# Optimization experiments

Hardware: AMD Instinct MI355X
Metric: run time of the kernel (lower is better)

Reference implementation:

```python
import math
import jax, jax.numpy as jnp
import numpy as np

D = 512
H = 8
HD = D // H
FF = 2048
EPS = 1e-5


def _layernorm(x, gamma, beta):
    mean = jnp.mean(x, axis=-1, keepdims=True)
    var = jnp.mean((x - mean) ** 2, axis=-1, keepdims=True)
    return gamma * (x - mean) / jnp.sqrt(var + EPS) + beta


def _attention(q, k, v, mask):
    # q,k,v: [B,H,Sq/Sk,hd]; mask: [B,Sq,Sk] additive, broadcast over heads
    scale = 1.0 / math.sqrt(q.shape[-1])
    scores = jnp.einsum('bhqd,bhkd->bhqk', q, k) * scale
    scores = scores + mask[:, None, :, :]
    probs = jax.nn.softmax(scores, axis=-1)
    return jnp.einsum('bhqk,bhkd->bhqd', probs, v)


def setup_inputs() -> dict:
    key = jax.random.key(0)
    ks = jax.random.split(key, 20)
    B, S_ENC, S_DEC = 256, 512, 64
    s = 0.02
    inp = {
        'x': jax.random.normal(ks[0], (B, S_ENC, D), jnp.float32),
        'y': jax.random.normal(ks[1], (B, S_DEC, D), jnp.float32),
        'mask': jnp.zeros((B, S_DEC, S_DEC), jnp.float32),
        'mask2': jnp.zeros((B, S_DEC, S_ENC), jnp.float32),
        # self-attention params
        'qkv_w': jax.random.normal(ks[2], (D, 3 * D), jnp.float32) * s,
        'qkv_b': jnp.zeros((3 * D,), jnp.float32),
        'sa_out_w': jax.random.normal(ks[3], (D, D), jnp.float32) * s,
        'sa_out_b': jnp.zeros((D,), jnp.float32),
        # cross-attention params
        'q_w': jax.random.normal(ks[4], (D, D), jnp.float32) * s,
        'q_b': jnp.zeros((D,), jnp.float32),
        'kv_w': jax.random.normal(ks[5], (D, 2 * D), jnp.float32) * s,
        'kv_b': jnp.zeros((2 * D,), jnp.float32),
        'ca_out_w': jax.random.normal(ks[6], (D, D), jnp.float32) * s,
        'ca_out_b': jnp.zeros((D,), jnp.float32),
        # ffn params
        'l1_w': jax.random.normal(ks[7], (D, FF), jnp.float32) * s,
        'l1_b': jnp.zeros((FF,), jnp.float32),
        'l2_w': jax.random.normal(ks[8], (FF, D), jnp.float32) * s,
        'l2_b': jnp.zeros((D,), jnp.float32),
        # layernorm params
        'g1': jnp.ones((D,), jnp.float32), 'b1': jnp.zeros((D,), jnp.float32),
        'g2': jnp.ones((D,), jnp.float32), 'b2': jnp.zeros((D,), jnp.float32),
        'g3': jnp.ones((D,), jnp.float32), 'b3': jnp.zeros((D,), jnp.float32),
    }
    return inp


def reference(x, y, mask, mask2, qkv_w, qkv_b, sa_out_w, sa_out_b,
              q_w, q_b, kv_w, kv_b, ca_out_w, ca_out_b,
              l1_w, l1_b, l2_w, l2_b, g1, b1, g2, b2, g3, b3):
    B, Sd, _ = y.shape
    Se = x.shape[1]

    # --- self attention (post-norm, dropout is identity at eval) ---
    resid = y
    qkv = y @ qkv_w + qkv_b                     # [B,Sd,3D]
    qkv = qkv.reshape(B, Sd, H, 3 * HD).transpose(0, 2, 1, 3)
    q, k, v = jnp.split(qkv, 3, axis=-1)        # each [B,H,Sd,hd]
    vals = _attention(q, k, v, mask)
    vals = vals.transpose(0, 2, 1, 3).reshape(B, Sd, D)
    y = vals @ sa_out_w + sa_out_b
    y = _layernorm(y + resid, g1, b1)

    # --- cross attention: kv from encoder x, q from decoder y ---
    resid = y
    kv = x @ kv_w + kv_b                        # [B,Se,2D]
    kv = kv.reshape(B, Se, H, 2 * HD).transpose(0, 2, 1, 3)
    k, v = jnp.split(kv, 2, axis=-1)            # each [B,H,Se,hd]
    q = (y @ q_w + q_b).reshape(B, Sd, H, HD).transpose(0, 2, 1, 3)
    vals = _attention(q, k, v, mask2)
    vals = vals.transpose(0, 2, 1, 3).reshape(B, Sd, D)
    y = vals @ ca_out_w + ca_out_b
    y = _layernorm(y + resid, g2, b2)

    # --- feed forward ---
    resid = y
    h = jax.nn.relu(y @ l1_w + l1_b)
    y = h @ l2_w + l2_b
    y = _layernorm(y + resid, g3, b3)
    return y
```

## Files before the change

### kernel.cpp

```cpp
#include <hip/hip_runtime.h>
#include <hip/hip_bf16.h>
#include <stdint.h>


#define SDEC 64
#define SENC 512
#define DMODEL 512
#define FFDIM 2048

typedef __bf16 bf16x8 __attribute__((ext_vector_type(8)));
typedef float  f32x4  __attribute__((ext_vector_type(4)));

static __device__ __forceinline__ float bf2f(unsigned short u) {
  union { unsigned int i; float f; } w; w.i = ((unsigned int)u) << 16; return w.f;
}
static __device__ __forceinline__ unsigned short f2bf(float f) {
  union { float f; unsigned int i; } w; w.f = f;
  unsigned int u = w.i;
  return (unsigned short)((u + 0x7fffu + ((u >> 16) & 1u)) >> 16);
}

static __device__ __forceinline__ void gl_lds16(const unsigned short* g, unsigned short* l) {
  __builtin_amdgcn_global_load_lds(
      (const __attribute__((address_space(1))) unsigned int*)g,
      (__attribute__((address_space(3))) unsigned int*)l,
      16, 0, 0);
}

__global__ __launch_bounds__(256)
void cvt_f32_bf16(const float* __restrict__ in, unsigned short* __restrict__ out, size_t n8)
{
  size_t i = (size_t)blockIdx.x * blockDim.x + threadIdx.x;
  const size_t stride = (size_t)gridDim.x * blockDim.x;
  for (; i < n8; i += stride) {
    const float* p = in + i * 8;
    float4 a = *(const float4*)p, b = *(const float4*)(p + 4);
    union { unsigned short s[8]; uint4 v; } u;
    u.s[0] = f2bf(a.x); u.s[1] = f2bf(a.y); u.s[2] = f2bf(a.z); u.s[3] = f2bf(a.w);
    u.s[4] = f2bf(b.x); u.s[5] = f2bf(b.y); u.s[6] = f2bf(b.z); u.s[7] = f2bf(b.w);
    *(uint4*)(out + i * 8) = u.v;
  }
}

template<int A_F32, int RELU, int OUT_F32>
__global__ __launch_bounds__(256, 2)
void gemm_kernel(const void* __restrict__ Aptr, const unsigned short* __restrict__ Bt,
                 const float* __restrict__ bias, void* __restrict__ Cptr,
                 int M, int N, int K)
{
  __shared__ unsigned short As[128 * 32];
  __shared__ unsigned short Bs[128 * 32];
  const int tid  = threadIdx.x;
  const int row0 = blockIdx.y * 128;
  const int col0 = blockIdx.x * 128;
  const int w    = tid >> 6, lane = tid & 63;
  const int wm   = w >> 1, wn = w & 1;
  const int gr   = lane >> 2;
  const int gc   = (lane & 3) * 8;
  const int srow = tid >> 2;
  const int scol = (tid & 3) * 8;

  f32x4 acc[4][4];
  #pragma unroll
  for (int i = 0; i < 4; ++i)
    #pragma unroll
    for (int j = 0; j < 4; ++j)
      acc[i][j] = (f32x4){0.f, 0.f, 0.f, 0.f};

  for (int k0 = 0; k0 < K; k0 += 32) {
    __syncthreads();
    if (A_F32) {
      const float* A = (const float*)Aptr;
      #pragma unroll
      for (int c = 0; c < 2; ++c) {
        const int r = srow + c * 64;
        const float* src = A + (size_t)(row0 + r) * K + (k0 + scol);
        float4 f0 = *(const float4*)src;
        float4 f1 = *(const float4*)(src + 4);
        union { unsigned short s[8]; uint4 v; } p;
        p.s[0] = f2bf(f0.x); p.s[1] = f2bf(f0.y); p.s[2] = f2bf(f0.z); p.s[3] = f2bf(f0.w);
        p.s[4] = f2bf(f1.x); p.s[5] = f2bf(f1.y); p.s[6] = f2bf(f1.z); p.s[7] = f2bf(f1.w);
        *(uint4*)&As[r * 32 + scol] = p.v;
      }
    } else {
      const unsigned short* A = (const unsigned short*)Aptr;
      #pragma unroll
      for (int i = 0; i < 2; ++i) {
        const int rbase = w * 32 + i * 16;
        gl_lds16(A + (size_t)(row0 + rbase + gr) * K + (k0 + gc), &As[rbase * 32]);
      }
    }
    #pragma unroll
    for (int i = 0; i < 2; ++i) {
      const int rbase = w * 32 + i * 16;
      gl_lds16(Bt + (size_t)(col0 + rbase + gr) * K + (k0 + gc), &Bs[rbase * 32]);
    }
    __syncthreads();

    const int fr = lane & 15, fk = (lane >> 4) * 8;
    bf16x8 af[4], bfr[4];
    #pragma unroll
    for (int mi = 0; mi < 4; ++mi)
      af[mi] = *(const bf16x8*)&As[(wm * 64 + mi * 16 + fr) * 32 + fk];
    #pragma unroll
    for (int ni = 0; ni < 4; ++ni)
      bfr[ni] = *(const bf16x8*)&Bs[(wn * 64 + ni * 16 + fr) * 32 + fk];
    #pragma unroll
    for (int mi = 0; mi < 4; ++mi)
      #pragma unroll
      for (int ni = 0; ni < 4; ++ni)
        acc[mi][ni] = __builtin_amdgcn_mfma_f32_16x16x32_bf16(af[mi], bfr[ni], acc[mi][ni], 0, 0, 0);
  }

  const int fr = lane & 15, fq = lane >> 4;
  #pragma unroll
  for (int ni = 0; ni < 4; ++ni) {
    const int c = col0 + wn * 64 + ni * 16 + fr;
    const float bv = bias ? bias[c] : 0.f;
    #pragma unroll
    for (int mi = 0; mi < 4; ++mi) {
      #pragma unroll
      for (int t = 0; t < 4; ++t) {
        const int r = row0 + wm * 64 + mi * 16 + fq * 4 + t;
        float v = acc[mi][ni][t] + bv;
        if (RELU) v = fmaxf(v, 0.f);
        if (OUT_F32) ((float*)Cptr)[(size_t)r * N + c] = v;
        else ((unsigned short*)Cptr)[(size_t)r * N + c] = f2bf(v);
      }
    }
  }
}

__global__ __launch_bounds__(256, 2)
void attn_mfma(const unsigned short* __restrict__ qbuf, int qstride, int qmul,
               const unsigned short* __restrict__ kvbuf, int kvstride, int kmul, int kadd,
               int tokmul, int Skv, const float* __restrict__ mask,
               unsigned short* __restrict__ vals, float scale)
{
  __shared__ unsigned short Qs[64 * 72];
  __shared__ unsigned short Ks[64 * 72];
  __shared__ unsigned short Vt[64 * 72];
  __shared__ unsigned short Ps[64 * 72];

  const int h = blockIdx.x, b = blockIdx.y;
  const int tid = threadIdx.x;
  const int w = tid >> 6, lane = tid & 63;
  const int srow = tid >> 2;
  const int sc0 = (tid & 3) * 16;

  {
    const unsigned short* qg = qbuf + (size_t)(b * 64 + srow) * qstride + h * qmul + sc0;
    *(uint4*)&Qs[srow * 72 + sc0]     = *(const uint4*)qg;
    *(uint4*)&Qs[srow * 72 + sc0 + 8] = *(const uint4*)(qg + 8);
  }

  const int fr = lane & 15;
  const int fg = lane >> 4;
  const int orow = fg * 4;

  float mstate[4], lstate[4];
  f32x4 oacc[4];
  #pragma unroll
  for (int t = 0; t < 4; ++t) { mstate[t] = -1e30f; lstate[t] = 0.f; }
  #pragma unroll
  for (int ni = 0; ni < 4; ++ni) oacc[ni] = (f32x4){0.f, 0.f, 0.f, 0.f};

  for (int j0 = 0; j0 < Skv; j0 += 64) {
    __syncthreads();
    {
      const unsigned short* kg = kvbuf + (size_t)(b * tokmul + j0 + srow) * kvstride
                                 + h * kmul + kadd + sc0;
      *(uint4*)&Ks[srow * 72 + sc0]     = *(const uint4*)kg;
      *(uint4*)&Ks[srow * 72 + sc0 + 8] = *(const uint4*)(kg + 8);
      const unsigned short* vg = kg + 64;
      uint4 v0 = *(const uint4*)vg;
      uint4 v1 = *(const uint4*)(vg + 8);
      const unsigned short* vsp = (const unsigned short*)&v0;
      #pragma unroll
      for (int jj = 0; jj < 8; ++jj) Vt[(sc0 + jj) * 72 + srow] = vsp[jj];
      vsp = (const unsigned short*)&v1;
      #pragma unroll
      for (int jj = 0; jj < 8; ++jj) Vt[(sc0 + 8 + jj) * 72 + srow] = vsp[jj];
    }
    __syncthreads();

    f32x4 s[4];
    #pragma unroll
    for (int ni = 0; ni < 4; ++ni) s[ni] = (f32x4){0.f, 0.f, 0.f, 0.f};
    #pragma unroll
    for (int ks = 0; ks < 2; ++ks) {
      bf16x8 aq = *(const bf16x8*)&Qs[(w * 16 + fr) * 72 + ks * 32 + fg * 8];
      #pragma unroll
      for (int ni = 0; ni < 4; ++ni) {
        bf16x8 bk = *(const bf16x8*)&Ks[(ni * 16 + fr) * 72 + ks * 32 + fg * 8];
        s[ni] = __builtin_amdgcn_mfma_f32_16x16x32_bf16(aq, bk, s[ni], 0, 0, 0);
      }
    }

    #pragma unroll
    for (int t = 0; t < 4; ++t) {
      const int grow = w * 16 + orow + t;
      const float* mrow = mask + ((size_t)b * 64 + grow) * Skv + j0;
      float sv[4];
      float tmax = -1e30f;
      #pragma unroll
      for (int ni = 0; ni < 4; ++ni) {
        sv[ni] = s[ni][t] * scale + mrow[ni * 16 + fr];
        tmax = fmaxf(tmax, sv[ni]);
      }
      #pragma unroll
      for (int off = 1; off < 16; off <<= 1) tmax = fmaxf(tmax, __shfl_xor(tmax, off));
      const float mn = fmaxf(mstate[t], tmax);
      const float fscl = __expf(mstate[t] - mn);
      mstate[t] = mn;
      float psum = 0.f;
      #pragma unroll
      for (int ni = 0; ni < 4; ++ni) {
        float p = __expf(sv[ni] - mn);
        psum += p;
        Ps[grow * 72 + ni * 16 + fr] = f2bf(p);
      }
      #pragma unroll
      for (int off = 1; off < 16; off <<= 1) psum += __shfl_xor(psum, off);
      lstate[t] = lstate[t] * fscl + psum;
      #pragma unroll
      for (int ni = 0; ni < 4; ++ni) oacc[ni][t] *= fscl;
    }
    __syncthreads();

    #pragma unroll
    for (int ks = 0; ks < 2; ++ks) {
      bf16x8 pa = *(const bf16x8*)&Ps[(w * 16 + fr) * 72 + ks * 32 + fg * 8];
      #pragma unroll
      for (int ni = 0; ni < 4; ++ni) {
        bf16x8 vb = *(const bf16x8*)&Vt[(ni * 16 + fr) * 72 + ks * 32 + fg * 8];
        oacc[ni] = __builtin_amdgcn_mfma_f32_16x16x32_bf16(pa, vb, oacc[ni], 0, 0, 0);
      }
    }
  }

  #pragma unroll
  for (int t = 0; t < 4; ++t) {
    const int grow = w * 16 + orow + t;
    const float inv = 1.f / lstate[t];
    unsigned short* og = vals + (size_t)(b * 64 + grow) * DMODEL + h * 64;
    #pragma unroll
    for (int ni = 0; ni < 4; ++ni)
      og[ni * 16 + fr] = f2bf(oacc[ni][t] * inv);
  }
}

__global__ __launch_bounds__(256)
void ln_kernel(const float* __restrict__ proj, const float* __restrict__ resid32,
               const unsigned short* __restrict__ resid16,
               const float* __restrict__ gamma, const float* __restrict__ beta,
               unsigned short* __restrict__ out16, float* __restrict__ out32)
{
  const int w = threadIdx.x >> 6, lane = threadIdx.x & 63;
  const size_t r = (size_t)blockIdx.x * 4 + w;
  const int d0 = lane * 8;

  float x[8];
  {
    const float* p = proj + r * DMODEL + d0;
    float4 a = *(const float4*)p, b = *(const float4*)(p + 4);
    x[0] = a.x; x[1] = a.y; x[2] = a.z; x[3] = a.w;
    x[4] = b.x; x[5] = b.y; x[6] = b.z; x[7] = b.w;
  }
  if (resid32) {
    const float* p = resid32 + r * DMODEL + d0;
    float4 a = *(const float4*)p, b = *(const float4*)(p + 4);
    x[0] += a.x; x[1] += a.y; x[2] += a.z; x[3] += a.w;
    x[4] += b.x; x[5] += b.y; x[6] += b.z; x[7] += b.w;
  } else {
    uint4 u = *(const uint4*)(resid16 + r * DMODEL + d0);
    const unsigned short* s = (const unsigned short*)&u;
    #pragma unroll
    for (int j = 0; j < 8; ++j) x[j] += bf2f(s[j]);
  }

  float sum = 0.f;
  #pragma unroll
  for (int j = 0; j < 8; ++j) sum += x[j];
  #pragma unroll
  for (int off = 32; off > 0; off >>= 1) sum += __shfl_xor(sum, off);
  const float mean = sum * (1.f / DMODEL);

  float vs = 0.f;
  #pragma unroll
  for (int j = 0; j < 8; ++j) { float t = x[j] - mean; vs += t * t; }
  #pragma unroll
  for (int off = 32; off > 0; off >>= 1) vs += __shfl_xor(vs, off);
  const float rstd = rsqrtf(vs * (1.f / DMODEL) + 1e-5f);

  float4 g0 = *(const float4*)(gamma + d0), g1 = *(const float4*)(gamma + d0 + 4);
  float4 b0 = *(const float4*)(beta + d0),  b1 = *(const float4*)(beta + d0 + 4);
  const float g[8]  = {g0.x, g0.y, g0.z, g0.w, g1.x, g1.y, g1.z, g1.w};
  const float bb[8] = {b0.x, b0.y, b0.z, b0.w, b1.x, b1.y, b1.z, b1.w};
  float y[8];
  #pragma unroll
  for (int j = 0; j < 8; ++j) y[j] = g[j] * (x[j] - mean) * rstd + bb[j];

  if (out16) {
    union { unsigned short s[8]; uint4 v; } p;
    #pragma unroll
    for (int j = 0; j < 8; ++j) p.s[j] = f2bf(y[j]);
    *(uint4*)(out16 + r * DMODEL + d0) = p.v;
  }
  if (out32) {
    float* o = out32 + r * DMODEL + d0;
    *(float4*)o       = (float4){y[0], y[1], y[2], y[3]};
    *(float4*)(o + 4) = (float4){y[4], y[5], y[6], y[7]};
  }
}

__global__ __launch_bounds__(256)
void transpose_cvt(const float* __restrict__ W, unsigned short* __restrict__ Wt,
                   int K, int N)
{
  __shared__ float tile[32][33];
  const int tx = threadIdx.x, ty = threadIdx.y;
  const int n = blockIdx.x * 32 + tx;
  #pragma unroll
  for (int rr = 0; rr < 4; ++rr) {
    const int k = blockIdx.y * 32 + ty + rr * 8;
    tile[ty + rr * 8][tx] = W[(size_t)k * N + n];
  }
  __syncthreads();
  const int k2 = blockIdx.y * 32 + tx;
  #pragma unroll
  for (int rr = 0; rr < 4; ++rr) {
    const int n2 = blockIdx.x * 32 + ty + rr * 8;
    Wt[(size_t)n2 * K + k2] = f2bf(tile[tx][ty + rr * 8]);
  }
}

extern "C" void kernel_launch(void* const* d_in, const int* in_sizes, int n_in,
                              void* d_out, int out_size, void* d_ws, size_t ws_size,
                              hipStream_t stream)
{
  const float* x        = (const float*)d_in[0];
  const float* y        = (const float*)d_in[1];
  const float* mask     = (const float*)d_in[2];
  const float* mask2    = (const float*)d_in[3];
  const float* qkv_w    = (const float*)d_in[4];
  const float* qkv_b    = (const float*)d_in[5];
  const float* sa_out_w = (const float*)d_in[6];
  const float* sa_out_b = (const float*)d_in[7];
  const float* q_w      = (const float*)d_in[8];
  const float* q_b      = (const float*)d_in[9];
  const float* kv_w     = (const float*)d_in[10];
  const float* kv_b     = (const float*)d_in[11];
  const float* ca_out_w = (const float*)d_in[12];
  const float* ca_out_b = (const float*)d_in[13];
  const float* l1_w     = (const float*)d_in[14];
  const float* l1_b     = (const float*)d_in[15];
  const float* l2_w     = (const float*)d_in[16];
  const float* l2_b     = (const float*)d_in[17];
  const float* g1 = (const float*)d_in[18];
  const float* b1 = (const float*)d_in[19];
  const float* g2 = (const float*)d_in[20];
  const float* b2 = (const float*)d_in[21];
  const float* g3 = (const float*)d_in[22];
  const float* b3 = (const float*)d_in[23];

  const int B  = in_sizes[1] / (SDEC * DMODEL);
  const int M  = B * SDEC;
  const int ME = B * SENC;

  char* ws = (char*)d_ws;
  size_t off = 0;
  auto alloc = [&](size_t bytes) -> char* {
    char* p = ws + off;
    off += (bytes + 255) & ~(size_t)255;
    return p;
  };
  unsigned short* qkv_wt = (unsigned short*)alloc((size_t)1536 * 512 * 2);
  unsigned short* sa_wt  = (unsigned short*)alloc((size_t)512 * 512 * 2);
  unsigned short* q_wt   = (unsigned short*)alloc((size_t)512 * 512 * 2);
  unsigned short* kv_wt  = (unsigned short*)alloc((size_t)1024 * 512 * 2);
  unsigned short* ca_wt  = (unsigned short*)alloc((size_t)512 * 512 * 2);
  unsigned short* l1_wt  = (unsigned short*)alloc((size_t)2048 * 512 * 2);
  unsigned short* l2_wt  = (unsigned short*)alloc((size_t)512 * 2048 * 2);
  unsigned short* kvb    = (unsigned short*)alloc((size_t)ME * 1024 * 2);
  char*           xreg   = alloc((size_t)ME * 512 * 2);
  unsigned short* xb     = (unsigned short*)xreg;
  unsigned short* qkvb   = (unsigned short*)xreg;
  unsigned short* qb     = (unsigned short*)xreg;
  unsigned short* y2b    = (unsigned short*)(xreg + (size_t)16777216);
  unsigned short* valsb  = (unsigned short*)(xreg + (size_t)50331648);
  float*          proj   = (float*)(xreg + (size_t)67108864);
  unsigned short* y1b    = (unsigned short*)(xreg + (size_t)100663296);
  unsigned short* hb     = kvb;
  (void)ws_size; (void)n_in; (void)out_size;

  dim3 tb(32, 8);
  transpose_cvt<<<dim3(1536 / 32, 512 / 32), tb, 0, stream>>>(qkv_w, qkv_wt, 512, 1536);
  transpose_cvt<<<dim3(512 / 32, 512 / 32), tb, 0, stream>>>(sa_out_w, sa_wt, 512, 512);
  transpose_cvt<<<dim3(512 / 32, 512 / 32), tb, 0, stream>>>(q_w, q_wt, 512, 512);
  transpose_cvt<<<dim3(1024 / 32, 512 / 32), tb, 0, stream>>>(kv_w, kv_wt, 512, 1024);
  transpose_cvt<<<dim3(512 / 32, 512 / 32), tb, 0, stream>>>(ca_out_w, ca_wt, 512, 512);
  transpose_cvt<<<dim3(2048 / 32, 512 / 32), tb, 0, stream>>>(l1_w, l1_wt, 512, 2048);
  transpose_cvt<<<dim3(512 / 32, 2048 / 32), tb, 0, stream>>>(l2_w, l2_wt, 2048, 512);

  const float scale = 0.125f;

  cvt_f32_bf16<<<4096, 256, 0, stream>>>(x, xb, (size_t)ME * 512 / 8);
  gemm_kernel<0, 0, 0><<<dim3(1024 / 128, ME / 128), 256, 0, stream>>>(xb, kv_wt, kv_b, kvb, ME, 1024, 512);

  gemm_kernel<1, 0, 0><<<dim3(1536 / 128, M / 128), 256, 0, stream>>>(y, qkv_wt, qkv_b, qkvb, M, 1536, 512);
  attn_mfma<<<dim3(8, B), 256, 0, stream>>>(qkvb, 1536, 192, qkvb, 1536, 192, 64, SDEC, SDEC, mask, valsb, scale);
  gemm_kernel<0, 0, 1><<<dim3(512 / 128, M / 128), 256, 0, stream>>>(valsb, sa_wt, sa_out_b, proj, M, 512, 512);
  ln_kernel<<<M / 4, 256, 0, stream>>>(proj, y, nullptr, g1, b1, y1b, nullptr);

  gemm_kernel<0, 0, 0><<<dim3(512 / 128, M / 128), 256, 0, stream>>>(y1b, q_wt, q_b, qb, M, 512, 512);
  attn_mfma<<<dim3(8, B), 256, 0, stream>>>(qb, 512, 64, kvb, 1024, 128, 0, SENC, SENC, mask2, valsb, scale);
  gemm_kernel<0, 0, 1><<<dim3(512 / 128, M / 128), 256, 0, stream>>>(valsb, ca_wt, ca_out_b, proj, M, 512, 512);
  ln_kernel<<<M / 4, 256, 0, stream>>>(proj, nullptr, y1b, g2, b2, y2b, nullptr);

  gemm_kernel<0, 1, 0><<<dim3(2048 / 128, M / 128), 256, 0, stream>>>(y2b, l1_wt, l1_b, hb, M, 2048, 512);
  gemm_kernel<0, 0, 1><<<dim3(512 / 128, M / 128), 256, 0, stream>>>(hb, l2_wt, l2_b, proj, M, 512, 2048);
  ln_kernel<<<M / 4, 256, 0, stream>>>(proj, nullptr, y2b, g3, b3, nullptr, (float*)d_out);
}
```

Measured before the change: 730.5 us.

## Double-buffer GEMM loads, swizzle workgroups, stage bf16 epilogue via LDS

The GEMM now double-buffers its LDS tiles, issuing the next K-slice's global-to-LDS loads before computing on the current one. Workgroups are remapped (XCD-style swizzle) in both the GEMM and attention kernels. The GEMM epilogue writes through LDS so global stores are coalesced 16-byte vectors. Projection outputs become bf16 instead of fp32, which halves traffic into the layernorm kernels but costs precision before the residual add and layernorm. The fp32-A path is dropped; y is converted to bf16 by a separate kernel.

```diff
diff --git a/kernel.cpp b/kernel.cpp
--- a/kernel.cpp
+++ b/kernel.cpp
@@ -42,23 +42,39 @@
   }
 }
 
-template<int A_F32, int RELU, int OUT_F32>
+template<int RELU>
 __global__ __launch_bounds__(256, 2)
-void gemm_kernel(const void* __restrict__ Aptr, const unsigned short* __restrict__ Bt,
-                 const float* __restrict__ bias, void* __restrict__ Cptr,
+void gemm_kernel(const unsigned short* __restrict__ A, const unsigned short* __restrict__ Bt,
+                 const float* __restrict__ bias, unsigned short* __restrict__ C,
                  int M, int N, int K)
 {
-  __shared__ unsigned short As[128 * 32];
-  __shared__ unsigned short Bs[128 * 32];
-  const int tid  = threadIdx.x;
-  const int row0 = blockIdx.y * 128;
-  const int col0 = blockIdx.x * 128;
-  const int w    = tid >> 6, lane = tid & 63;
-  const int wm   = w >> 1, wn = w & 1;
-  const int gr   = lane >> 2;
-  const int gc   = (lane & 3) * 8;
-  const int srow = tid >> 2;
-  const int scol = (tid & 3) * 8;
+  __shared__ unsigned short sh[4 * 128 * 32];
+  const int tid = threadIdx.x;
+
+  const int gx   = gridDim.x;
+  const int nwg  = gx * gridDim.y;
+  const int orig = blockIdx.y * gx + blockIdx.x;
+  const int wg   = (orig & 7) * (nwg >> 3) + (orig >> 3);
+  const int row0 = (wg / gx) * 128;
+  const int col0 = (wg % gx) * 128;
+
+  const int w = tid >> 6, lane = tid & 63;
+  const int wm = w >> 1, wn = w & 1;
+  const int gr = lane >> 2, gc = (lane & 3) * 8;
+
+  unsigned short* As0 = sh;
+  unsigned short* Bs0 = sh + 8192;
+
+  auto STAGE = [&](int k0, int buf) {
+    unsigned short* as = As0 + buf * 4096;
+    unsigned short* bs = Bs0 + buf * 4096;
+    #pragma unroll
+    for (int i = 0; i < 2; ++i) {
+      const int rbase = w * 32 + i * 16;
+      gl_lds16(A  + (size_t)(row0 + rbase + gr) * K + (k0 + gc), as + rbase * 32);
+      gl_lds16(Bt + (size_t)(col0 + rbase + gr) * K + (k0 + gc), bs + rbase * 32);
+    }
+  };
 
   f32x4 acc[4][4];
   #pragma unroll
@@ -67,66 +83,81 @@
     for (int j = 0; j < 4; ++j)
       acc[i][j] = (f32x4){0.f, 0.f, 0.f, 0.f};
 
-  for (int k0 = 0; k0 < K; k0 += 32) {
-    __syncthreads();
-    if (A_F32) {
-      const float* A = (const float*)Aptr;
-      #pragma unroll
-      for (int c = 0; c < 2; ++c) {
-        const int r = srow + c * 64;
-        const float* src = A + (size_t)(row0 + r) * K + (k0 + scol);
-        float4 f0 = *(const float4*)src;
-        float4 f1 = *(const float4*)(src + 4);
-        union { unsigned short s[8]; uint4 v; } p;
-        p.s[0] = f2bf(f0.x); p.s[1] = f2bf(f0.y); p.s[2] = f2bf(f0.z); p.s[3] = f2bf(f0.w);
-        p.s[4] = f2bf(f1.x); p.s[5] = f2bf(f1.y); p.s[6] = f2bf(f1.z); p.s[7] = f2bf(f1.w);
-        *(uint4*)&As[r * 32 + scol] = p.v;
-      }
-    } else {
-      const unsigned short* A = (const unsigned short*)Aptr;
-      #pragma unroll
-      for (int i = 0; i < 2; ++i) {
-        const int rbase = w * 32 + i * 16;
-        gl_lds16(A + (size_t)(row0 + rbase + gr) * K + (k0 + gc), &As[rbase * 32]);
-      }
-    }
-    #pragma unroll
-    for (int i = 0; i < 2; ++i) {
-      const int rbase = w * 32 + i * 16;
-      gl_lds16(Bt + (size_t)(col0 + rbase + gr) * K + (k0 + gc), &Bs[rbase * 32]);
-    }
-    __syncthreads();
-
-    const int fr = lane & 15, fk = (lane >> 4) * 8;
+  const int fr = lane & 15, fk = (lane >> 4) * 8;
+
+  STAGE(0, 0);
+  int cur = 0;
+  for (int k0 = 0; k0 + 32 < K; k0 += 32) {
+    STAGE(k0 + 32, cur ^ 1);
+    asm volatile("s_waitcnt vmcnt(4)" ::: "memory");
+    __builtin_amdgcn_s_barrier();
+    asm volatile("" ::: "memory");
+    {
+      const unsigned short* as = As0 + cur * 4096;
+      const unsigned short* bs = Bs0 + cur * 4096;
+      bf16x8 af[4], bfr[4];
+      #pragma unroll
+      for (int mi = 0; mi < 4; ++mi)
+        af[mi] = *(const bf16x8*)&as[(wm * 64 + mi * 16 + fr) * 32 + fk];
+      #pragma unroll
+      for (int ni = 0; ni < 4; ++ni)
+        bfr[ni] = *(const bf16x8*)&bs[(wn * 64 + ni * 16 + fr) * 32 + fk];
+      #pragma unroll
+      for (int mi = 0; mi < 4; ++mi)
+        #pragma unroll
+        for (int ni = 0; ni < 4; ++ni)
+          acc[mi][ni] = __builtin_amdgcn_mfma_f32_16x16x32_bf16(af[mi], bfr[ni], acc[mi][ni], 0, 0, 0);
+    }
+    asm volatile("" ::: "memory");
+    __builtin_amdgcn_s_barrier();
+    cur ^= 1;
+  }
+  asm volatile("s_waitcnt vmcnt(0)" ::: "memory");
+  __builtin_amdgcn_s_barrier();
+  asm volatile("" ::: "memory");
+  {
+    const unsigned short* as = As0 + cur * 4096;
+    const unsigned short* bs = Bs0 + cur * 4096;
     bf16x8 af[4], bfr[4];
     #pragma unroll
     for (int mi = 0; mi < 4; ++mi)
-      af[mi] = *(const bf16x8*)&As[(wm * 64 + mi * 16 + fr) * 32 + fk];
+      af[mi] = *(const bf16x8*)&as[(wm * 64 + mi * 16 + fr) * 32 + fk];
     #pragma unroll
     for (int ni = 0; ni < 4; ++ni)
-      bfr[ni] = *(const bf16x8*)&Bs[(wn * 64 + ni * 16 + fr) * 32 + fk];
+      bfr[ni] = *(const bf16x8*)&bs[(wn * 64 + ni * 16 + fr) * 32 + fk];
     #pragma unroll
     for (int mi = 0; mi < 4; ++mi)
       #pragma unroll
       for (int ni = 0; ni < 4; ++ni)
         acc[mi][ni] = __builtin_amdgcn_mfma_f32_16x16x32_bf16(af[mi], bfr[ni], acc[mi][ni], 0, 0, 0);
   }
-
-  const int fr = lane & 15, fq = lane >> 4;
-  #pragma unroll
-  for (int ni = 0; ni < 4; ++ni) {
-    const int c = col0 + wn * 64 + ni * 16 + fr;
-    const float bv = bias ? bias[c] : 0.f;
-    #pragma unroll
-    for (int mi = 0; mi < 4; ++mi) {
-      #pragma unroll
-      for (int t = 0; t < 4; ++t) {
-        const int r = row0 + wm * 64 + mi * 16 + fq * 4 + t;
-        float v = acc[mi][ni][t] + bv;
-        if (RELU) v = fmaxf(v, 0.f);
-        if (OUT_F32) ((float*)Cptr)[(size_t)r * N + c] = v;
-        else ((unsigned short*)Cptr)[(size_t)r * N + c] = f2bf(v);
+  asm volatile("" ::: "memory");
+  __builtin_amdgcn_s_barrier();
+
+  {
+    const int fq = lane >> 4;
+    #pragma unroll
+    for (int ni = 0; ni < 4; ++ni) {
+      const int c = wn * 64 + ni * 16 + fr;
+      const float bv = bias ? bias[col0 + c] : 0.f;
+      #pragma unroll
+      for (int mi = 0; mi < 4; ++mi) {
+        #pragma unroll
+        for (int t = 0; t < 4; ++t) {
+          const int r = wm * 64 + mi * 16 + fq * 4 + t;
+          float v = acc[mi][ni][t] + bv;
+          if (RELU) v = fmaxf(v, 0.f);
+          sh[r * 128 + c] = f2bf(v);
+        }
       }
+    }
+    __syncthreads();
+    const int rr = tid >> 4;
+    const int cc = (tid & 15) * 8;
+    #pragma unroll
+    for (int p = 0; p < 8; ++p) {
+      const int r = p * 16 + rr;
+      *(uint4*)(C + (size_t)(row0 + r) * N + col0 + cc) = *(const uint4*)&sh[r * 128 + cc];
     }
   }
 }
@@ -142,7 +173,11 @@
   __shared__ unsigned short Vt[64 * 72];
   __shared__ unsigned short Ps[64 * 72];
 
-  const int h = blockIdx.x, b = blockIdx.y;
+  const int nwg  = gridDim.x * gridDim.y;
+  const int orig = blockIdx.y * gridDim.x + blockIdx.x;
+  const int wg   = (orig & 7) * (nwg >> 3) + (orig >> 3);
+  const int h = wg & 7, b = wg >> 3;
+
   const int tid = threadIdx.x;
   const int w = tid >> 6, lane = tid & 63;
   const int srow = tid >> 2;
@@ -251,7 +286,7 @@
 }
 
 __global__ __launch_bounds__(256)
-void ln_kernel(const float* __restrict__ proj, const float* __restrict__ resid32,
+void ln_kernel(const unsigned short* __restrict__ proj16, const float* __restrict__ resid32,
                const unsigned short* __restrict__ resid16,
                const float* __restrict__ gamma, const float* __restrict__ beta,
                unsigned short* __restrict__ out16, float* __restrict__ out32)
@@ -262,10 +297,10 @@
 
   float x[8];
   {
-    const float* p = proj + r * DMODEL + d0;
-    float4 a = *(const float4*)p, b = *(const float4*)(p + 4);
-    x[0] = a.x; x[1] = a.y; x[2] = a.z; x[3] = a.w;
-    x[4] = b.x; x[5] = b.y; x[6] = b.z; x[7] = b.w;
+    uint4 u = *(const uint4*)(proj16 + r * DMODEL + d0);
+    const unsigned short* s = (const unsigned short*)&u;
+    #pragma unroll
+    for (int j = 0; j < 8; ++j) x[j] = bf2f(s[j]);
   }
   if (resid32) {
     const float* p = resid32 + r * DMODEL + d0;
@@ -389,8 +424,9 @@
   unsigned short* qb     = (unsigned short*)xreg;
   unsigned short* y2b    = (unsigned short*)(xreg + (size_t)16777216);
   unsigned short* valsb  = (unsigned short*)(xreg + (size_t)50331648);
-  float*          proj   = (float*)(xreg + (size_t)67108864);
+  unsigned short* proj   = (unsigned short*)(xreg + (size_t)67108864);
   unsigned short* y1b    = (unsigned short*)(xreg + (size_t)100663296);
+  unsigned short* yb     = (unsigned short*)(xreg + (size_t)117440512);
   unsigned short* hb     = kvb;
   (void)ws_size; (void)n_in; (void)out_size;
 
@@ -406,19 +442,20 @@
   const float scale = 0.125f;
 
   cvt_f32_bf16<<<4096, 256, 0, stream>>>(x, xb, (size_t)ME * 512 / 8);
-  gemm_kernel<0, 0, 0><<<dim3(1024 / 128, ME / 128), 256, 0, stream>>>(xb, kv_wt, kv_b, kvb, ME, 1024, 512);
-
-  gemm_kernel<1, 0, 0><<<dim3(1536 / 128, M / 128), 256, 0, stream>>>(y, qkv_wt, qkv_b, qkvb, M, 1536, 512);
+  gemm_kernel<0><<<dim3(1024 / 128, ME / 128), 256, 0, stream>>>(xb, kv_wt, kv_b, kvb, ME, 1024, 512);
+
+  cvt_f32_bf16<<<4096, 256, 0, stream>>>(y, yb, (size_t)M * 512 / 8);
+  gemm_kernel<0><<<dim3(1536 / 128, M / 128), 256, 0, stream>>>(yb, qkv_wt, qkv_b, qkvb, M, 1536, 512);
   attn_mfma<<<dim3(8, B), 256, 0, stream>>>(qkvb, 1536, 192, qkvb, 1536, 192, 64, SDEC, SDEC, mask, valsb, scale);
-  gemm_kernel<0, 0, 1><<<dim3(512 / 128, M / 128), 256, 0, stream>>>(valsb, sa_wt, sa_out_b, proj, M, 512, 512);
+  gemm_kernel<0><<<dim3(512 / 128, M / 128), 256, 0, stream>>>(valsb, sa_wt, sa_out_b, proj, M, 512, 512);
   ln_kernel<<<M / 4, 256, 0, stream>>>(proj, y, nullptr, g1, b1, y1b, nullptr);
 
-  gemm_kernel<0, 0, 0><<<dim3(512 / 128, M / 128), 256, 0, stream>>>(y1b, q_wt, q_b, qb, M, 512, 512);
+  gemm_kernel<0><<<dim3(512 / 128, M / 128), 256, 0, stream>>>(y1b, q_wt, q_b, qb, M, 512, 512);
   attn_mfma<<<dim3(8, B), 256, 0, stream>>>(qb, 512, 64, kvb, 1024, 128, 0, SENC, SENC, mask2, valsb, scale);
-  gemm_kernel<0, 0, 1><<<dim3(512 / 128, M / 128), 256, 0, stream>>>(valsb, ca_wt, ca_out_b, proj, M, 512, 512);
+  gemm_kernel<0><<<dim3(512 / 128, M / 128), 256, 0, stream>>>(valsb, ca_wt, ca_out_b, proj, M, 512, 512);
   ln_kernel<<<M / 4, 256, 0, stream>>>(proj, nullptr, y1b, g2, b2, y2b, nullptr);
 
-  gemm_kernel<0, 1, 0><<<dim3(2048 / 128, M / 128), 256, 0, stream>>>(y2b, l1_wt, l1_b, hb, M, 2048, 512);
-  gemm_kernel<0, 0, 1><<<dim3(512 / 128, M / 128), 256, 0, stream>>>(hb, l2_wt, l2_b, proj, M, 512, 2048);
+  gemm_kernel<1><<<dim3(2048 / 128, M / 128), 256, 0, stream>>>(y2b, l1_wt, l1_b, hb, M, 2048, 512);
+  gemm_kernel<0><<<dim3(512 / 128, M / 128), 256, 0, stream>>>(hb, l2_wt, l2_b, proj, M, 512, 2048);
   ln_kernel<<<M / 4, 256, 0, stream>>>(proj, nullptr, y2b, g3, b3, nullptr, (float*)d_out);
 }
```

New measurement: 616.3 us. 15.6% less time.
